# Kernel tuning notes

Measured on AMD Instinct MI355X. Metric: run time of the kernel, lower is better.

The kernel has to match this reference:

```python
import jax, jax.numpy as jnp
import numpy as np

E, R, CIN, COUT = 8, 8, 256, 256
B, H, W = 16, 64, 64
DN = ('NCHW', 'OIHW', 'NCHW')


def setup_inputs() -> dict:
    key = jax.random.key(0)
    k1, k2, k3, k4 = jax.random.split(key, 4)
    x = jax.random.normal(k1, (B, CIN, H, W), jnp.float32)
    probs = jax.nn.softmax(jax.random.normal(k2, (E,), jnp.float32))
    # in conv: rank filters over in_channels, kernel (1,3); out conv: kernel (3,1)
    weight_in = jax.random.normal(k3, (E, R, CIN, 1, 3), jnp.float32) * 0.02
    weight_out = jax.random.normal(k4, (E, COUT, R, 3, 1), jnp.float32) * 0.02
    return {"x": x, "probs": probs, "weight_in": weight_in, "weight_out": weight_out}


def _expert_conv(x, w_in, w_out):
    # in conv: stride (1,1), padding (0,1) -> [B,R,H,W]
    h = jax.lax.conv_general_dilated(x, w_in, window_strides=(1, 1),
                                     padding=[(0, 0), (1, 1)], dimension_numbers=DN)
    # out conv: stride (1,1), padding (1,0) -> [B,COUT,H,W]
    return jax.lax.conv_general_dilated(h, w_out, window_strides=(1, 1),
                                        padding=[(1, 1), (0, 0)], dimension_numbers=DN)


def reference(x, probs, weight_in, weight_out):
    # vmap over experts replaces the Python loop; outs: [E,B,COUT,H,W]
    outs = jax.vmap(lambda wi, wo: _expert_conv(x, wi, wo))(weight_in, weight_out)
    # probability-weighted sum over experts (stack + sum in the original)
    return jnp.einsum('e,ebchw->bchw', probs, outs)
```

## Files before the change

### kernel.cpp

```cpp
#include <hip/hip_runtime.h>
#include <hip/hip_bf16.h>


typedef __bf16 bf16x8 __attribute__((ext_vector_type(8)));
typedef float  f32x4  __attribute__((ext_vector_type(4)));
typedef unsigned short us8 __attribute__((ext_vector_type(8)));

#define CIN_  256
#define COUT_ 256
#define M1    64
#define K1    768
#define K2    192

static __device__ __forceinline__ unsigned short f2bf(float f) {
    union { float f; unsigned u; } v; v.f = f;
    unsigned r = v.u + 0x7FFFu + ((v.u >> 16) & 1u);
    return (unsigned short)(r >> 16);
}

__global__ void prep_weights(const float* __restrict__ probs,
                             const float* __restrict__ w_in,
                             const float* __restrict__ w_out,
                             unsigned short* __restrict__ W1,
                             unsigned short* __restrict__ W2) {
    int idx = blockIdx.x * blockDim.x + threadIdx.x;
    if (idx < M1 * K1) {
        int er = idx / K1, rem = idx % K1;
        int kx = rem / CIN_, c = rem % CIN_;
        int e = er >> 3;
        float v = probs[e] * w_in[(er * CIN_ + c) * 3 + kx];
        W1[idx] = f2bf(v);
    } else {
        int i2 = idx - M1 * K1;
        if (i2 < COUT_ * K2) {
            int o = i2 / K2, rem = i2 % K2;
            int ky = rem / M1, er = rem % M1;
            int e = er >> 3, r = er & 7;
            float v = w_out[((e * COUT_ + o) * 8 + r) * 3 + ky];
            W2[i2] = f2bf(v);
        }
    }
}

#define XS_STRIDE 40
__global__ __launch_bounds__(256)
void conv_in_kernel(const float* __restrict__ x,
                    const unsigned short* __restrict__ W1,
                    unsigned short* __restrict__ h) {
    __shared__ unsigned short xs[66 * XS_STRIDE];
    const int bid  = blockIdx.x;
    const int b    = bid >> 6, y = bid & 63;
    const int tid  = threadIdx.x;
    const int lane = tid & 63;
    const int wave = tid >> 6;
    const int g    = lane >> 4;
    const int lr   = lane & 15;

    if (tid < 64) {
        int ns = (tid < 32) ? 0 : 65;
        xs[ns * XS_STRIDE + (tid & 31)] = 0;
    }

    f32x4 acc[4];
    #pragma unroll
    for (int i = 0; i < 4; ++i) acc[i] = (f32x4){0.f, 0.f, 0.f, 0.f};

    const int c_l = tid & 31;
    const int n0  = (tid >> 5) << 3;
    const float* xrow = x + (((b * CIN_ + c_l) * 64 + y) * 64 + n0);

    for (int cc = 0; cc < 8; ++cc) {
        __syncthreads();
        float4 v0 = *(const float4*)(xrow + cc * 32 * 4096);
        float4 v1 = *(const float4*)(xrow + cc * 32 * 4096 + 4);
        unsigned short* dst = &xs[(n0 + 1) * XS_STRIDE + c_l];
        dst[0 * XS_STRIDE] = f2bf(v0.x);
        dst[1 * XS_STRIDE] = f2bf(v0.y);
        dst[2 * XS_STRIDE] = f2bf(v0.z);
        dst[3 * XS_STRIDE] = f2bf(v0.w);
        dst[4 * XS_STRIDE] = f2bf(v1.x);
        dst[5 * XS_STRIDE] = f2bf(v1.y);
        dst[6 * XS_STRIDE] = f2bf(v1.z);
        dst[7 * XS_STRIDE] = f2bf(v1.w);
        __syncthreads();
        #pragma unroll
        for (int kx = 0; kx < 3; ++kx) {
            bf16x8 afrag = *(const bf16x8*)(W1 + (wave * 16 + lr) * K1 +
                                            kx * CIN_ + cc * 32 + g * 8);
            #pragma unroll
            for (int nt = 0; nt < 4; ++nt) {
                int ns = nt * 16 + lr + kx;
                bf16x8 bfrag = *(const bf16x8*)&xs[ns * XS_STRIDE + g * 8];
                acc[nt] = __builtin_amdgcn_mfma_f32_16x16x32_bf16(afrag, bfrag,
                                                                  acc[nt], 0, 0, 0);
            }
        }
    }
    #pragma unroll
    for (int nt = 0; nt < 4; ++nt) {
        int n = nt * 16 + lr;
        #pragma unroll
        for (int r2 = 0; r2 < 4; ++r2) {
            int m = wave * 16 + g * 4 + r2;
            h[((b * M1 + m) * 64 + y) * 64 + n] = f2bf(acc[nt][r2]);
        }
    }
}

#define HS_STRIDE 200
__global__ __launch_bounds__(256)
void conv_out_kernel(const unsigned short* __restrict__ h,
                     const unsigned short* __restrict__ W2,
                     float* __restrict__ out) {
    __shared__ unsigned short hs[64 * HS_STRIDE];
    const int bid  = blockIdx.x;
    const int b    = bid >> 6, y = bid & 63;
    const int tid  = threadIdx.x;
    const int lane = tid & 63;
    const int wave = tid >> 6;
    const int g    = lane >> 4;
    const int lr   = lane & 15;

    const int ms = tid >> 2;
    const int x0 = (tid & 3) << 4;
    const int sw = (tid & 3) << 3;
    #pragma unroll
    for (int ky = 0; ky < 3; ++ky) {
        int ys = y + ky - 1;
        int kcol = ky * M1 + ms;
        int kswz = kcol ^ sw;
        if (ys >= 0 && ys < 64) {
            const unsigned short* src = h + ((b * M1 + ms) * 64 + ys) * 64 + x0;
            us8 v0 = *(const us8*)(src);
            us8 v1 = *(const us8*)(src + 8);
            #pragma unroll
            for (int i = 0; i < 8; ++i)
                hs[(x0 + i) * HS_STRIDE + kswz] = v0[i];
            #pragma unroll
            for (int i = 0; i < 8; ++i)
                hs[(x0 + 8 + i) * HS_STRIDE + kswz] = v1[i];
        } else {
            #pragma unroll
            for (int i = 0; i < 16; ++i)
                hs[(x0 + i) * HS_STRIDE + kswz] = 0;
        }
    }
    __syncthreads();

    f32x4 acc[4][4];
    #pragma unroll
    for (int ot = 0; ot < 4; ++ot)
        #pragma unroll
        for (int nt = 0; nt < 4; ++nt) acc[ot][nt] = (f32x4){0.f, 0.f, 0.f, 0.f};

    #pragma unroll
    for (int kc = 0; kc < 6; ++kc) {
        bf16x8 bfrag[4];
        #pragma unroll
        for (int nt = 0; nt < 4; ++nt) {
            int xr = nt * 16 + lr;
            bfrag[nt] = *(const bf16x8*)&hs[xr * HS_STRIDE + kc * 32 + ((g ^ nt) << 3)];
        }
        #pragma unroll
        for (int ot = 0; ot < 4; ++ot) {
            bf16x8 afrag = *(const bf16x8*)(W2 + ((wave * 4 + ot) * 16 + lr) * K2 +
                                            kc * 32 + g * 8);
            #pragma unroll
            for (int nt = 0; nt < 4; ++nt)
                acc[ot][nt] = __builtin_amdgcn_mfma_f32_16x16x32_bf16(afrag, bfrag[nt],
                                                                      acc[ot][nt], 0, 0, 0);
        }
    }

    #pragma unroll
    for (int ot = 0; ot < 4; ++ot) {
        #pragma unroll
        for (int r2 = 0; r2 < 4; ++r2) {
            int o = (wave * 4 + ot) * 16 + g * 4 + r2;
            float* orow = out + ((b * COUT_ + o) * 64 + y) * 64;
            #pragma unroll
            for (int nt = 0; nt < 4; ++nt)
                orow[nt * 16 + lr] = acc[ot][nt][r2];
        }
    }
}

extern "C" void kernel_launch(void* const* d_in, const int* in_sizes, int n_in,
                              void* d_out, int out_size, void* d_ws, size_t ws_size,
                              hipStream_t stream) {
    const float* x     = (const float*)d_in[0];
    const float* probs = (const float*)d_in[1];
    const float* w_in  = (const float*)d_in[2];
    const float* w_out = (const float*)d_in[3];
    float* out = (float*)d_out;

    unsigned short* W1 = (unsigned short*)d_ws;
    unsigned short* W2 = W1 + M1 * K1;
    unsigned short* h  = W2 + COUT_ * K2;

    prep_weights<<<(M1 * K1 + COUT_ * K2 + 255) / 256, 256, 0, stream>>>(
        probs, w_in, w_out, W1, W2);
    conv_in_kernel<<<16 * 64, 256, 0, stream>>>(x, W1, h);
    conv_out_kernel<<<16 * 64, 256, 0, stream>>>(h, W2, out);
}
```

Measured before the change: 56.91 us.

## Store intermediate in padded channel-last layout and stage full input row once

The intermediate h is now written transposed ([b][y+1][x][r], with zeroed top/bottom padding rows) so the out-conv can copy contiguous 128-byte rows straight into shared memory instead of doing scattered 2-byte transposing stores with swizzling. The in-conv loads all 256 channels of an input row up front into a larger LDS tile with vectorized bf16 stores, removing the per-chunk double barriers. The prep kernel also zeros the padding rows. This costs more LDS and registers in the in-conv and drops the swizzle, which may bring back bank conflicts on the B-fragment reads.

```diff
diff --git a/kernel.cpp b/kernel.cpp
--- a/kernel.cpp
+++ b/kernel.cpp
@@ -3,14 +3,17 @@
 
 
 typedef __bf16 bf16x8 __attribute__((ext_vector_type(8)));
+typedef __bf16 bf16x4 __attribute__((ext_vector_type(4)));
 typedef float  f32x4  __attribute__((ext_vector_type(4)));
-typedef unsigned short us8 __attribute__((ext_vector_type(8)));
+typedef float  f32x4v __attribute__((ext_vector_type(4)));
 
 #define CIN_  256
 #define COUT_ 256
 #define M1    64
 #define K1    768
 #define K2    192
+#define CS    264
+#define HS    200
 
 static __device__ __forceinline__ unsigned short f2bf(float f) {
     union { float f; unsigned u; } v; v.f = f;
@@ -22,32 +25,39 @@
                              const float* __restrict__ w_in,
                              const float* __restrict__ w_out,
                              unsigned short* __restrict__ W1,
-                             unsigned short* __restrict__ W2) {
+                             unsigned short* __restrict__ W2,
+                             unsigned short* __restrict__ hT) {
     int idx = blockIdx.x * blockDim.x + threadIdx.x;
     if (idx < M1 * K1) {
         int er = idx / K1, rem = idx % K1;
         int kx = rem / CIN_, c = rem % CIN_;
         int e = er >> 3;
-        float v = probs[e] * w_in[(er * CIN_ + c) * 3 + kx];
-        W1[idx] = f2bf(v);
-    } else {
+        W1[idx] = f2bf(probs[e] * w_in[(er * CIN_ + c) * 3 + kx]);
+    } else if (idx < 2 * M1 * K1) {
         int i2 = idx - M1 * K1;
-        if (i2 < COUT_ * K2) {
-            int o = i2 / K2, rem = i2 % K2;
+        int o = i2 / K2, rem = i2 % K2;
+        if (rem < K2) {
             int ky = rem / M1, er = rem % M1;
             int e = er >> 3, r = er & 7;
-            float v = w_out[((e * COUT_ + o) * 8 + r) * 3 + ky];
-            W2[i2] = f2bf(v);
-        }
-    }
-}
-
-#define XS_STRIDE 40
+            W2[i2] = f2bf(w_out[((e * COUT_ + o) * 8 + r) * 3 + ky]);
+        }
+    } else {
+        int i3 = idx - 2 * M1 * K1;
+        if (i3 < 16384) {
+            int b = i3 >> 10, r = i3 & 1023;
+            int yp = (r >> 9) * 65;
+            int col = (r & 511) * 8;
+            bf16x8 z = {};
+            *(bf16x8*)(hT + ((b * 66 + yp) * 4096) + col) = z;
+        }
+    }
+}
+
 __global__ __launch_bounds__(256)
 void conv_in_kernel(const float* __restrict__ x,
                     const unsigned short* __restrict__ W1,
-                    unsigned short* __restrict__ h) {
-    __shared__ unsigned short xs[66 * XS_STRIDE];
+                    unsigned short* __restrict__ hT) {
+    __shared__ unsigned short xs[66 * CS];
     const int bid  = blockIdx.x;
     const int b    = bid >> 6, y = bid & 63;
     const int tid  = threadIdx.x;
@@ -56,63 +66,66 @@
     const int g    = lane >> 4;
     const int lr   = lane & 15;
 
-    if (tid < 64) {
-        int ns = (tid < 32) ? 0 : 65;
-        xs[ns * XS_STRIDE + (tid & 31)] = 0;
-    }
+    if (tid < 66) {
+        int row = (tid < 33) ? 0 : 65;
+        int col = (tid - (tid < 33 ? 0 : 33)) * 8;
+        bf16x4 z4 = {};
+        *(bf16x4*)&xs[row * CS + col] = z4;
+        *(bf16x4*)&xs[row * CS + col + 4] = z4;
+    }
+
+    const int cb = tid & 31;
+    const int n0 = (tid >> 5) << 3;
+    const float* xp = x + (((b * CIN_ + cb * 8) * 64 + y) * 64 + n0);
+    f32x4v va[8], vb[8];
+    #pragma unroll
+    for (int i = 0; i < 8; ++i) {
+        va[i] = *(const f32x4v*)(xp + i * 4096);
+        vb[i] = *(const f32x4v*)(xp + i * 4096 + 4);
+    }
+    #pragma unroll
+    for (int j = 0; j < 4; ++j) {
+        bf16x8 r0, r1;
+        #pragma unroll
+        for (int i = 0; i < 8; ++i) { r0[i] = (__bf16)va[i][j]; r1[i] = (__bf16)vb[i][j]; }
+        *(bf16x8*)&xs[(n0 + j + 1) * CS + cb * 8] = r0;
+        *(bf16x8*)&xs[(n0 + j + 5) * CS + cb * 8] = r1;
+    }
+    __syncthreads();
 
     f32x4 acc[4];
     #pragma unroll
     for (int i = 0; i < 4; ++i) acc[i] = (f32x4){0.f, 0.f, 0.f, 0.f};
 
-    const int c_l = tid & 31;
-    const int n0  = (tid >> 5) << 3;
-    const float* xrow = x + (((b * CIN_ + c_l) * 64 + y) * 64 + n0);
-
+    const unsigned short* w1p = W1 + (wave * 16 + lr) * K1 + g * 8;
+    #pragma unroll
     for (int cc = 0; cc < 8; ++cc) {
-        __syncthreads();
-        float4 v0 = *(const float4*)(xrow + cc * 32 * 4096);
-        float4 v1 = *(const float4*)(xrow + cc * 32 * 4096 + 4);
-        unsigned short* dst = &xs[(n0 + 1) * XS_STRIDE + c_l];
-        dst[0 * XS_STRIDE] = f2bf(v0.x);
-        dst[1 * XS_STRIDE] = f2bf(v0.y);
-        dst[2 * XS_STRIDE] = f2bf(v0.z);
-        dst[3 * XS_STRIDE] = f2bf(v0.w);
-        dst[4 * XS_STRIDE] = f2bf(v1.x);
-        dst[5 * XS_STRIDE] = f2bf(v1.y);
-        dst[6 * XS_STRIDE] = f2bf(v1.z);
-        dst[7 * XS_STRIDE] = f2bf(v1.w);
-        __syncthreads();
         #pragma unroll
         for (int kx = 0; kx < 3; ++kx) {
-            bf16x8 afrag = *(const bf16x8*)(W1 + (wave * 16 + lr) * K1 +
-                                            kx * CIN_ + cc * 32 + g * 8);
+            bf16x8 af = *(const bf16x8*)(w1p + kx * CIN_ + cc * 32);
             #pragma unroll
             for (int nt = 0; nt < 4; ++nt) {
-                int ns = nt * 16 + lr + kx;
-                bf16x8 bfrag = *(const bf16x8*)&xs[ns * XS_STRIDE + g * 8];
-                acc[nt] = __builtin_amdgcn_mfma_f32_16x16x32_bf16(afrag, bfrag,
-                                                                  acc[nt], 0, 0, 0);
+                bf16x8 bf = *(const bf16x8*)&xs[(nt * 16 + lr + kx) * CS + cc * 32 + g * 8];
+                acc[nt] = __builtin_amdgcn_mfma_f32_16x16x32_bf16(af, bf, acc[nt], 0, 0, 0);
             }
         }
     }
+    unsigned short* hp = hT + ((b * 66 + y + 1) * 64) * 64;
     #pragma unroll
     for (int nt = 0; nt < 4; ++nt) {
         int n = nt * 16 + lr;
-        #pragma unroll
-        for (int r2 = 0; r2 < 4; ++r2) {
-            int m = wave * 16 + g * 4 + r2;
-            h[((b * M1 + m) * 64 + y) * 64 + n] = f2bf(acc[nt][r2]);
-        }
-    }
-}
-
-#define HS_STRIDE 200
+        bf16x4 pk;
+        #pragma unroll
+        for (int r2 = 0; r2 < 4; ++r2) pk[r2] = (__bf16)acc[nt][r2];
+        *(bf16x4*)&hp[n * 64 + wave * 16 + g * 4] = pk;
+    }
+}
+
 __global__ __launch_bounds__(256)
-void conv_out_kernel(const unsigned short* __restrict__ h,
+void conv_out_kernel(const unsigned short* __restrict__ hT,
                      const unsigned short* __restrict__ W2,
                      float* __restrict__ out) {
-    __shared__ unsigned short hs[64 * HS_STRIDE];
+    __shared__ unsigned short hs[64 * HS];
     const int bid  = blockIdx.x;
     const int b    = bid >> 6, y = bid & 63;
     const int tid  = threadIdx.x;
@@ -121,29 +134,13 @@
     const int g    = lane >> 4;
     const int lr   = lane & 15;
 
-    const int ms = tid >> 2;
-    const int x0 = (tid & 3) << 4;
-    const int sw = (tid & 3) << 3;
-    #pragma unroll
-    for (int ky = 0; ky < 3; ++ky) {
-        int ys = y + ky - 1;
-        int kcol = ky * M1 + ms;
-        int kswz = kcol ^ sw;
-        if (ys >= 0 && ys < 64) {
-            const unsigned short* src = h + ((b * M1 + ms) * 64 + ys) * 64 + x0;
-            us8 v0 = *(const us8*)(src);
-            us8 v1 = *(const us8*)(src + 8);
-            #pragma unroll
-            for (int i = 0; i < 8; ++i)
-                hs[(x0 + i) * HS_STRIDE + kswz] = v0[i];
-            #pragma unroll
-            for (int i = 0; i < 8; ++i)
-                hs[(x0 + 8 + i) * HS_STRIDE + kswz] = v1[i];
-        } else {
-            #pragma unroll
-            for (int i = 0; i < 16; ++i)
-                hs[(x0 + i) * HS_STRIDE + kswz] = 0;
-        }
+    if (tid < 192) {
+        int ky = tid >> 6, xr = tid & 63;
+        const unsigned short* src = hT + (((b * 66) + y + ky) * 64 + xr) * 64;
+        unsigned short* dst = &hs[xr * HS + ky * 64];
+        #pragma unroll
+        for (int j = 0; j < 8; ++j)
+            *(bf16x8*)&dst[j * 8] = *(const bf16x8*)&src[j * 8];
     }
     __syncthreads();
 
@@ -157,17 +154,15 @@
     for (int kc = 0; kc < 6; ++kc) {
         bf16x8 bfrag[4];
         #pragma unroll
-        for (int nt = 0; nt < 4; ++nt) {
-            int xr = nt * 16 + lr;
-            bfrag[nt] = *(const bf16x8*)&hs[xr * HS_STRIDE + kc * 32 + ((g ^ nt) << 3)];
-        }
+        for (int nt = 0; nt < 4; ++nt)
+            bfrag[nt] = *(const bf16x8*)&hs[(nt * 16 + lr) * HS + kc * 32 + g * 8];
         #pragma unroll
         for (int ot = 0; ot < 4; ++ot) {
-            bf16x8 afrag = *(const bf16x8*)(W2 + ((wave * 4 + ot) * 16 + lr) * K2 +
-                                            kc * 32 + g * 8);
+            bf16x8 af = *(const bf16x8*)(W2 + ((wave * 4 + ot) * 16 + lr) * K2 +
+                                         kc * 32 + g * 8);
             #pragma unroll
             for (int nt = 0; nt < 4; ++nt)
-                acc[ot][nt] = __builtin_amdgcn_mfma_f32_16x16x32_bf16(afrag, bfrag[nt],
+                acc[ot][nt] = __builtin_amdgcn_mfma_f32_16x16x32_bf16(af, bfrag[nt],
                                                                       acc[ot][nt], 0, 0, 0);
         }
     }
@@ -196,10 +191,10 @@
 
     unsigned short* W1 = (unsigned short*)d_ws;
     unsigned short* W2 = W1 + M1 * K1;
-    unsigned short* h  = W2 + COUT_ * K2;
-
-    prep_weights<<<(M1 * K1 + COUT_ * K2 + 255) / 256, 256, 0, stream>>>(
-        probs, w_in, w_out, W1, W2);
-    conv_in_kernel<<<16 * 64, 256, 0, stream>>>(x, W1, h);
-    conv_out_kernel<<<16 * 64, 256, 0, stream>>>(h, W2, out);
-}
+    unsigned short* hT = W2 + COUT_ * K2;
+
+    prep_weights<<<(2 * M1 * K1 + 16384 + 255) / 256, 256, 0, stream>>>(
+        probs, w_in, w_out, W1, W2, hT);
+    conv_in_kernel<<<16 * 64, 256, 0, stream>>>(x, W1, hT);
+    conv_out_kernel<<<16 * 64, 256, 0, stream>>>(hT, W2, out);
+}
```

After: 57.83 us. No clear change (+1.6%).
